# Kernel tuning notes

Measured on AMD Instinct MI355X. Metric: run time of the kernel, lower is better.

## Reference

```python
import jax, jax.numpy as jnp
import numpy as np

N = 50000
E = 800000
F_IN = 64
HID = 64
NCLS = 16


def setup_inputs() -> dict:
    key = jax.random.key(0)
    ks = jax.random.split(key, 8)
    x = jax.random.normal(ks[0], (N, F_IN), dtype=jnp.float32)
    edge_index = jax.random.randint(ks[1], (2, E), 0, N, dtype=jnp.int64)
    edge_weight = jax.random.uniform(ks[2], (E,), dtype=jnp.float32)
    # GCNConv glorot-style weights (PyG stores weight as [in, out]) and zero bias
    W1 = jax.random.normal(ks[3], (F_IN, HID), dtype=jnp.float32) * (1.0 / np.sqrt(F_IN))
    b1 = jnp.zeros((HID,), dtype=jnp.float32)
    W2 = jax.random.normal(ks[4], (HID, HID), dtype=jnp.float32) * (1.0 / np.sqrt(HID))
    b2 = jnp.zeros((HID,), dtype=jnp.float32)
    Wout = jax.random.normal(ks[5], (HID, NCLS), dtype=jnp.float32) * (1.0 / np.sqrt(HID))
    bout = jnp.zeros((NCLS,), dtype=jnp.float32)
    return {"x": x, "edge_index": edge_index, "edge_weight": edge_weight,
            "W1": W1, "b1": b1, "W2": W2, "b2": b2, "Wout": Wout, "bout": bout}


def _gcn_norm(edge_index, edge_weight, num_nodes):
    # PyG gcn_norm with add_self_loops=True (self-loop weight = 1.0)
    row = jnp.concatenate([edge_index[0], jnp.arange(num_nodes, dtype=edge_index.dtype)])
    col = jnp.concatenate([edge_index[1], jnp.arange(num_nodes, dtype=edge_index.dtype)])
    w = jnp.concatenate([edge_weight, jnp.ones((num_nodes,), dtype=edge_weight.dtype)])
    deg = jax.ops.segment_sum(w, col, num_segments=num_nodes)  # [N]
    dinv = jnp.where(deg > 0, jax.lax.rsqrt(deg), 0.0)
    norm = dinv[row] * w * dinv[col]  # [E+N]
    return row, col, norm


def _gcn_conv(h, row, col, norm, W, b, num_nodes):
    h = h @ W                                   # [N, out]
    msg = h[row] * norm[:, None]                # gather + scale, [E+N, out]
    out = jax.ops.segment_sum(msg, col, num_segments=num_nodes)  # scatter-add
    return out + b


def reference(x, edge_index, edge_weight, W1, b1, W2, b2, Wout, bout):
    num_nodes = x.shape[0]
    row, col, norm = _gcn_norm(edge_index, edge_weight, num_nodes)
    h = _gcn_conv(x, row, col, norm, W1, b1, num_nodes)
    h = jax.nn.relu(h)  # dropout is identity in eval mode
    h = _gcn_conv(h, row, col, norm, W2, b2, num_nodes)
    h = jax.nn.relu(h)
    logits = h @ Wout + bout
    return jax.nn.softmax(logits, axis=1)
```

## Files before the change

### kernel.cpp

```cpp
#include <hip/hip_runtime.h>
#include <math.h>

#define NN 50000
#define NE 800000
#define F 64
#define NCLS 16

#define BKS 7
#define BKN 128
#define NBK 391
#define CAP 2560
#define B1C 4096
#define B1B 196
#define CAP2 3072

typedef unsigned short u16;
typedef __attribute__((ext_vector_type(8))) unsigned short ushort8v;

__device__ __forceinline__ float bf2f(u16 h) {
    return __uint_as_float((unsigned)h << 16);
}
__device__ __forceinline__ u16 f2bf(float f) {
    unsigned u = __float_as_uint(f);
    return (u16)((u + 0x7fffu + ((u >> 16) & 1u)) >> 16);
}

__global__ void k_init_cur(int* __restrict__ cur) {
    int b = blockIdx.x * 256 + threadIdx.x;
    if (b < NBK) cur[b] = b * CAP;
}


__global__ __launch_bounds__(512) void k_bucket1(const int* __restrict__ row,
                                                 const int* __restrict__ col,
                                                 const float* __restrict__ w,
                                                 int* __restrict__ bkcur,
                                                 int2* __restrict__ tmp) {
    __shared__ int hist[512];
    __shared__ int sa[512], sb[512];
    __shared__ int lbase[512];
    __shared__ int gbase[512];
    __shared__ int lcur[512];
    __shared__ int2 stage[B1C];
    int t = threadIdx.x;
    int e0 = blockIdx.x * B1C;
    int cnt = min(B1C, NE - e0);
    hist[t] = 0;
    __syncthreads();

    int mykey[8]; int myb[8]; int myw[8]; bool myv[8];
#pragma unroll
    for (int k = 0; k < 8; ++k) {
        int i = t + k * 512;
        myv[k] = (i < cnt);
        if (myv[k]) {
            int e = e0 + i;
            int c = col[e];
            myb[k]   = c >> BKS;
            mykey[k] = (row[e] << BKS) | (c & (BKN - 1));
            myw[k]   = __float_as_int(w[e]);
            atomicAdd(&hist[myb[k]], 1);
        }
    }
    __syncthreads();

    sa[t] = hist[t];
    __syncthreads();
    int* src = sa; int* dst = sb;
#pragma unroll
    for (int off = 1; off < 512; off <<= 1) {
        dst[t] = src[t] + ((t >= off) ? src[t - off] : 0);
        __syncthreads();
        int* tq = src; src = dst; dst = tq;
    }
    int lex = src[t] - hist[t];
    lbase[t] = lex;
    lcur[t]  = lex;
    gbase[t] = (t < NBK && hist[t] > 0) ? atomicAdd(&bkcur[t], hist[t]) : 0;
    __syncthreads();

#pragma unroll
    for (int k = 0; k < 8; ++k) {
        if (myv[k]) {
            int pos = atomicAdd(&lcur[myb[k]], 1);
            stage[pos] = make_int2(mykey[k], myw[k]);
        }
    }
    __syncthreads();

    for (int i = t; i < cnt; i += 512) {
        int lo = 0, hi = NBK;
        while (hi - lo > 1) {
            int mid = (lo + hi) >> 1;
            if (lbase[mid] <= i) lo = mid; else hi = mid;
        }
        tmp[gbase[lo] + (i - lbase[lo])] = stage[i];
    }
}


__global__ __launch_bounds__(256) void k_bucket2(const int* __restrict__ bkcur,
                                                 const int2* __restrict__ tmp,
                                                 int2* __restrict__ sedge,
                                                 int* __restrict__ begA,
                                                 int* __restrict__ endA,
                                                 float* __restrict__ dinv) {
    __shared__ int2 stage[CAP2];
    __shared__ int2 sorted[CAP2];
    __shared__ int hist[BKN];
    __shared__ int sa[BKN], sb[BKN];
    __shared__ int lcur[BKN];
    int b = blockIdx.x;
    int t = threadIdx.x;
    int rbeg = b * CAP;
    int cnt = min(bkcur[b] - rbeg, CAP2);
    if (t < BKN) hist[t] = 0;
    __syncthreads();
    for (int i = t; i < cnt; i += 256) {
        int2 ed = tmp[rbeg + i];
        stage[i] = ed;
        atomicAdd(&hist[ed.x & (BKN - 1)], 1);
    }
    __syncthreads();
    if (t < BKN) sa[t] = hist[t];
    __syncthreads();
    int* src = sa; int* dst = sb;
#pragma unroll
    for (int off = 1; off < BKN; off <<= 1) {
        if (t < BKN) dst[t] = src[t] + ((t >= off) ? src[t - off] : 0);
        __syncthreads();
        int* tq = src; src = dst; dst = tq;
    }
    int node0 = b * BKN;
    int lincl = 0, lexcl = 0;
    if (t < BKN) {
        lincl = src[t];
        lexcl = lincl - hist[t];
        lcur[t] = lexcl;
        if (node0 + t < NN) {
            begA[node0 + t] = rbeg + lexcl;
            endA[node0 + t] = rbeg + lincl;
        }
    }
    __syncthreads();
    for (int i = t; i < cnt; i += 256) {
        int2 ed = stage[i];
        int pos = atomicAdd(&lcur[ed.x & (BKN - 1)], 1);
        sorted[pos] = ed;
    }
    __syncthreads();
    if (t < BKN && node0 + t < NN) {
        float s = 1.0f;
        for (int e = lexcl; e < lincl; ++e) s += __int_as_float(sorted[e].y);
        dinv[node0 + t] = rsqrtf(s);
    }
    for (int i = t; i < cnt; i += 256) {
        int2 ed = sorted[i];
        sedge[rbeg + i] = make_int2(ed.x >> BKS, ed.y);
    }
}


template<bool BF>
__global__ __launch_bounds__(256) void k_mm64(const void* __restrict__ Xv,
                                              const float* __restrict__ W,
                                              u16* __restrict__ Y) {
    __shared__ float sW[64 * 64];
    __shared__ float sX[16][64];
    int tid = threadIdx.x;
    int c  = tid & 63;
    int wv = tid >> 6;
    for (int i = tid; i < 64 * 64; i += 256) sW[i] = W[i];
    int r0 = blockIdx.x * 16;
#pragma unroll
    for (int i = tid; i < 16 * 64; i += 256) {
        size_t idx = (size_t)(r0 + (i >> 6)) * 64 + (i & 63);
        if (BF) sX[i >> 6][i & 63] = bf2f(((const u16*)Xv)[idx]);
        else    sX[i >> 6][i & 63] = ((const float*)Xv)[idx];
    }
    __syncthreads();
    int rb = wv * 4;
    float a0 = 0.f, a1 = 0.f, a2 = 0.f, a3 = 0.f;
#pragma unroll
    for (int k = 0; k < 64; k += 4) {
        float4 x0 = *(const float4*)&sX[rb + 0][k];
        float4 x1 = *(const float4*)&sX[rb + 1][k];
        float4 x2 = *(const float4*)&sX[rb + 2][k];
        float4 x3 = *(const float4*)&sX[rb + 3][k];
        float wA = sW[(k + 0) * 64 + c];
        float wB = sW[(k + 1) * 64 + c];
        float wC = sW[(k + 2) * 64 + c];
        float wD = sW[(k + 3) * 64 + c];
        a0 += x0.x * wA + x0.y * wB + x0.z * wC + x0.w * wD;
        a1 += x1.x * wA + x1.y * wB + x1.z * wC + x1.w * wD;
        a2 += x2.x * wA + x2.y * wB + x2.z * wC + x2.w * wD;
        a3 += x3.x * wA + x3.y * wB + x3.z * wC + x3.w * wD;
    }
    Y[(size_t)(r0 + rb + 0) * 64 + c] = f2bf(a0);
    Y[(size_t)(r0 + rb + 1) * 64 + c] = f2bf(a1);
    Y[(size_t)(r0 + rb + 2) * 64 + c] = f2bf(a2);
    Y[(size_t)(r0 + rb + 3) * 64 + c] = f2bf(a3);
}


template<bool HEAD>
__global__ __launch_bounds__(256) void k_agg(const u16* __restrict__ A,
                                             const int* __restrict__ begA,
                                             const int* __restrict__ endA,
                                             const int2* __restrict__ sedge,
                                             const float* __restrict__ dinv,
                                             const float* __restrict__ bias,
                                             u16* __restrict__ B,
                                             const float* __restrict__ Wout,
                                             const float* __restrict__ bout,
                                             float* __restrict__ out) {
    __shared__ float sWout[64 * NCLS];
    __shared__ float sh[8][64];
    int tid  = threadIdx.x;
    int wv   = tid >> 6;
    int lane = tid & 63;
    int half = lane >> 5;
    int sub  = lane & 31;
    int slot = sub >> 3;
    int fg   = sub & 7;
    int node = blockIdx.x * 8 + wv * 2 + half;
    if (HEAD) {
        for (int i = tid; i < 64 * NCLS; i += 256) sWout[i] = Wout[i];
    }
    int beg = begA[node];
    int deg = endA[node] - beg;
    float acc[8] = {0.f, 0.f, 0.f, 0.f, 0.f, 0.f, 0.f, 0.f};
    for (int base = 0; base < deg; base += 32) {
        int i = base + sub;
        int2 ed = (i < deg) ? sedge[beg + i] : make_int2(0, 0);
        float nmr = __int_as_float(ed.y) * dinv[ed.x];
        int m = min(32, deg - base);
        int steps = (m + 3) >> 2;
        for (int t = 0; t < steps; ++t) {
            int idx = (half << 5) + (t << 2) + slot;
            int   s  = __shfl(ed.x, idx);
            float nm = __shfl(nmr, idx);
            const ushort8v a = *(const ushort8v*)(A + (size_t)s * 64 + (fg << 3));
#pragma unroll
            for (int j = 0; j < 8; ++j) acc[j] += bf2f(a[j]) * nm;
        }
    }
#pragma unroll
    for (int o = 8; o <= 16; o <<= 1) {
#pragma unroll
        for (int j = 0; j < 8; ++j) acc[j] += __shfl_xor(acc[j], o);
    }
    if (slot == 0) {
        float d = dinv[node];
        float d2 = d * d;
        const ushort8v self = *(const ushort8v*)(A + (size_t)node * 64 + (fg << 3));
        const float4 bb0 = *(const float4*)(bias + (fg << 3));
        const float4 bb1 = *(const float4*)(bias + (fg << 3) + 4);
        float bbv[8] = {bb0.x, bb0.y, bb0.z, bb0.w, bb1.x, bb1.y, bb1.z, bb1.w};
        ushort8v ov;
#pragma unroll
        for (int j = 0; j < 8; ++j) {
            float v = fmaxf(acc[j] * d + bf2f(self[j]) * d2 + bbv[j], 0.f);
            ov[j] = f2bf(v);
            if (HEAD) sh[wv * 2 + half][(fg << 3) + j] = v;
        }
        *(ushort8v*)(B + (size_t)node * 64 + (fg << 3)) = ov;
    }
    if (HEAD) {
        __syncthreads();
        int nib  = tid >> 5;
        int sub2 = tid & 31;
        int c = sub2 & 15, q = sub2 >> 4;
        const float* hrow = sh[nib];
        float p = 0.f;
#pragma unroll
        for (int k = 0; k < 32; ++k)
            p += hrow[q * 32 + k] * sWout[(q * 32 + k) * NCLS + c];
        p += __shfl_xor(p, 16);
        p += bout[c];
        float mx = p;
#pragma unroll
        for (int o = 8; o >= 1; o >>= 1) mx = fmaxf(mx, __shfl_xor(mx, o, 16));
        float ex = expf(p - mx);
        float s = ex;
#pragma unroll
        for (int o = 8; o >= 1; o >>= 1) s += __shfl_xor(s, o, 16);
        if (q == 0) out[(size_t)(blockIdx.x * 8 + nib) * NCLS + c] = ex / s;
    }
}


extern "C" void kernel_launch(void* const* d_in, const int* in_sizes, int n_in,
                              void* d_out, int out_size, void* d_ws, size_t ws_size,
                              hipStream_t stream) {
    const float* x    = (const float*)d_in[0];
    const int*   ei   = (const int*)d_in[1];
    const float* ew   = (const float*)d_in[2];
    const float* W1   = (const float*)d_in[3];
    const float* b1   = (const float*)d_in[4];
    const float* W2   = (const float*)d_in[5];
    const float* b2   = (const float*)d_in[6];
    const float* Wout = (const float*)d_in[7];
    const float* bout = (const float*)d_in[8];
    const int* row = ei;
    const int* col = ei + NE;

    int*   ip     = (int*)d_ws;
    int*   begA   = ip;
    int*   endA   = ip + 50048;
    float* dinv   = (float*)(ip + 100096);
    int*   bkcur  = ip + 150144;
    int2*  sedge  = (int2*)(ip + 150656);
    u16*   A      = (u16*)(ip + 150656 + 2 * NBK * CAP);
    u16*   B      = A + 3200000;
    int2*  tmp    = (int2*)A;

    k_init_cur<<<2, 256, 0, stream>>>(bkcur);
    k_bucket1<<<B1B, 512, 0, stream>>>(row, col, ew, bkcur, tmp);
    k_bucket2<<<NBK, 256, 0, stream>>>(bkcur, tmp, sedge, begA, endA, dinv);

    k_mm64<false><<<NN / 16, 256, 0, stream>>>(x, W1, A);
    k_agg<false><<<NN / 8, 256, 0, stream>>>(A, begA, endA, sedge, dinv, b1, B,
                                             nullptr, nullptr, nullptr);
    k_mm64<true><<<NN / 16, 256, 0, stream>>>(B, W2, A);
    k_agg<true><<<NN / 8, 256, 0, stream>>>(A, begA, endA, sedge, dinv, b2, B,
                                            Wout, bout, (float*)d_out);
}
```

Measured before the change: 188.2 us.

## Fuse first-layer matmul into edge bucketing kernel and peel first aggregation chunk

```diff
diff --git a/kernel.cpp b/kernel.cpp
--- a/kernel.cpp
+++ b/kernel.cpp
@@ -12,6 +12,7 @@
 #define CAP 2560
 #define B1C 4096
 #define B1B 196
+#define MMB 1563
 #define CAP2 3072
 
 typedef unsigned short u16;
@@ -31,70 +32,112 @@
 }
 
 
-__global__ __launch_bounds__(512) void k_bucket1(const int* __restrict__ row,
+__global__ __launch_bounds__(512) void k_sort_mm(const int* __restrict__ row,
                                                  const int* __restrict__ col,
                                                  const float* __restrict__ w,
                                                  int* __restrict__ bkcur,
-                                                 int2* __restrict__ tmp) {
-    __shared__ int hist[512];
-    __shared__ int sa[512], sb[512];
-    __shared__ int lbase[512];
-    __shared__ int gbase[512];
-    __shared__ int lcur[512];
-    __shared__ int2 stage[B1C];
+                                                 int2* __restrict__ tmp,
+                                                 const float* __restrict__ X,
+                                                 const float* __restrict__ W,
+                                                 u16* __restrict__ Y) {
+    __shared__ __align__(16) char smem[53248];
     int t = threadIdx.x;
-    int e0 = blockIdx.x * B1C;
-    int cnt = min(B1C, NE - e0);
-    hist[t] = 0;
-    __syncthreads();
-
-    int mykey[8]; int myb[8]; int myw[8]; bool myv[8];
-#pragma unroll
-    for (int k = 0; k < 8; ++k) {
-        int i = t + k * 512;
-        myv[k] = (i < cnt);
-        if (myv[k]) {
-            int e = e0 + i;
-            int c = col[e];
-            myb[k]   = c >> BKS;
-            mykey[k] = (row[e] << BKS) | (c & (BKN - 1));
-            myw[k]   = __float_as_int(w[e]);
-            atomicAdd(&hist[myb[k]], 1);
-        }
-    }
-    __syncthreads();
-
-    sa[t] = hist[t];
-    __syncthreads();
-    int* src = sa; int* dst = sb;
-#pragma unroll
-    for (int off = 1; off < 512; off <<= 1) {
-        dst[t] = src[t] + ((t >= off) ? src[t - off] : 0);
-        __syncthreads();
-        int* tq = src; src = dst; dst = tq;
-    }
-    int lex = src[t] - hist[t];
-    lbase[t] = lex;
-    lcur[t]  = lex;
-    gbase[t] = (t < NBK && hist[t] > 0) ? atomicAdd(&bkcur[t], hist[t]) : 0;
-    __syncthreads();
-
-#pragma unroll
-    for (int k = 0; k < 8; ++k) {
-        if (myv[k]) {
-            int pos = atomicAdd(&lcur[myb[k]], 1);
-            stage[pos] = make_int2(mykey[k], myw[k]);
-        }
-    }
-    __syncthreads();
-
-    for (int i = t; i < cnt; i += 512) {
-        int lo = 0, hi = NBK;
-        while (hi - lo > 1) {
-            int mid = (lo + hi) >> 1;
-            if (lbase[mid] <= i) lo = mid; else hi = mid;
-        }
-        tmp[gbase[lo] + (i - lbase[lo])] = stage[i];
+    if (blockIdx.x < B1B) {
+        int*  hist   = (int*)smem;
+        int*  sa     = hist + 512;
+        int*  sb     = sa + 512;
+        int*  lbase  = sb + 512;
+        int*  gbase  = lbase + 512;
+        int*  lcur   = gbase + 512;
+        u16*  stageB = (u16*)(lcur + 512);
+        int2* stage  = (int2*)(stageB + 4096);
+
+        int e0 = blockIdx.x * B1C;
+        int cnt = min(B1C, NE - e0);
+        hist[t] = 0;
+        __syncthreads();
+
+        int mykey[8]; int myb[8]; int myw[8]; bool myv[8];
+#pragma unroll
+        for (int k = 0; k < 8; ++k) {
+            int i = t + k * 512;
+            myv[k] = (i < cnt);
+            if (myv[k]) {
+                int e = e0 + i;
+                int c = col[e];
+                myb[k]   = c >> BKS;
+                mykey[k] = (row[e] << BKS) | (c & (BKN - 1));
+                myw[k]   = __float_as_int(w[e]);
+                atomicAdd(&hist[myb[k]], 1);
+            }
+        }
+        __syncthreads();
+
+        sa[t] = hist[t];
+        __syncthreads();
+        int* src = sa; int* dst = sb;
+#pragma unroll
+        for (int off = 1; off < 512; off <<= 1) {
+            dst[t] = src[t] + ((t >= off) ? src[t - off] : 0);
+            __syncthreads();
+            int* tq = src; src = dst; dst = tq;
+        }
+        int lex = src[t] - hist[t];
+        lbase[t] = lex;
+        lcur[t]  = lex;
+        gbase[t] = (t < NBK && hist[t] > 0) ? atomicAdd(&bkcur[t], hist[t]) : 0;
+        __syncthreads();
+
+#pragma unroll
+        for (int k = 0; k < 8; ++k) {
+            if (myv[k]) {
+                int pos = atomicAdd(&lcur[myb[k]], 1);
+                stage[pos]  = make_int2(mykey[k], myw[k]);
+                stageB[pos] = (u16)myb[k];
+            }
+        }
+        __syncthreads();
+
+        for (int i = t; i < cnt; i += 512) {
+            int b = stageB[i];
+            tmp[gbase[b] + (i - lbase[b])] = stage[i];
+        }
+    } else {
+        float* sW = (float*)smem;
+        float (*sX)[64] = (float(*)[64])(smem + 16384);
+        for (int i = t; i < 64 * 64; i += 512) sW[i] = W[i];
+        int r0 = (blockIdx.x - B1B) * 32;
+        for (int i = t; i < 32 * 64; i += 512) {
+            int rr = i >> 6, cc = i & 63;
+            int r = r0 + rr;
+            sX[rr][cc] = (r < NN) ? X[(size_t)r * 64 + cc] : 0.f;
+        }
+        __syncthreads();
+        int c  = t & 63;
+        int wv = t >> 6;
+        int rb = wv * 4;
+        float a0 = 0.f, a1 = 0.f, a2 = 0.f, a3 = 0.f;
+#pragma unroll
+        for (int k = 0; k < 64; k += 4) {
+            float4 x0 = *(const float4*)&sX[rb + 0][k];
+            float4 x1 = *(const float4*)&sX[rb + 1][k];
+            float4 x2 = *(const float4*)&sX[rb + 2][k];
+            float4 x3 = *(const float4*)&sX[rb + 3][k];
+            float wA = sW[(k + 0) * 64 + c];
+            float wB = sW[(k + 1) * 64 + c];
+            float wC = sW[(k + 2) * 64 + c];
+            float wD = sW[(k + 3) * 64 + c];
+            a0 += x0.x * wA + x0.y * wB + x0.z * wC + x0.w * wD;
+            a1 += x1.x * wA + x1.y * wB + x1.z * wC + x1.w * wD;
+            a2 += x2.x * wA + x2.y * wB + x2.z * wC + x2.w * wD;
+            a3 += x3.x * wA + x3.y * wB + x3.z * wC + x3.w * wD;
+        }
+        float av[4] = {a0, a1, a2, a3};
+#pragma unroll
+        for (int k = 0; k < 4; ++k) {
+            int r = r0 + rb + k;
+            if (r < NN) Y[(size_t)r * 64 + c] = f2bf(av[k]);
+        }
     }
 }
 
@@ -161,10 +204,9 @@
 }
 
 
-template<bool BF>
-__global__ __launch_bounds__(256) void k_mm64(const void* __restrict__ Xv,
-                                              const float* __restrict__ W,
-                                              u16* __restrict__ Y) {
+__global__ __launch_bounds__(256) void k_mm64b(const u16* __restrict__ Xv,
+                                               const float* __restrict__ W,
+                                               u16* __restrict__ Y) {
     __shared__ float sW[64 * 64];
     __shared__ float sX[16][64];
     int tid = threadIdx.x;
@@ -175,8 +217,7 @@
 #pragma unroll
     for (int i = tid; i < 16 * 64; i += 256) {
         size_t idx = (size_t)(r0 + (i >> 6)) * 64 + (i & 63);
-        if (BF) sX[i >> 6][i & 63] = bf2f(((const u16*)Xv)[idx]);
-        else    sX[i >> 6][i & 63] = ((const float*)Xv)[idx];
+        sX[i >> 6][i & 63] = bf2f(Xv[idx]);
     }
     __syncthreads();
     int rb = wv * 4;
@@ -230,7 +271,24 @@
     int beg = begA[node];
     int deg = endA[node] - beg;
     float acc[8] = {0.f, 0.f, 0.f, 0.f, 0.f, 0.f, 0.f, 0.f};
-    for (int base = 0; base < deg; base += 32) {
+
+    {
+        int2 ed = (sub < deg) ? sedge[beg + sub] : make_int2(0, 0);
+        float nmr = __int_as_float(ed.y) * dinv[ed.x];
+        int mval = min(32, deg);
+#pragma unroll
+        for (int t = 0; t < 8; ++t) {
+            if ((t << 2) < mval) {
+                int idx = (half << 5) + (t << 2) + slot;
+                int   s  = __shfl(ed.x, idx);
+                float nm = __shfl(nmr, idx);
+                const ushort8v a = *(const ushort8v*)(A + (size_t)s * 64 + (fg << 3));
+#pragma unroll
+                for (int j = 0; j < 8; ++j) acc[j] += bf2f(a[j]) * nm;
+            }
+        }
+    }
+    for (int base = 32; base < deg; base += 32) {
         int i = base + sub;
         int2 ed = (i < deg) ? sedge[beg + i] : make_int2(0, 0);
         float nmr = __int_as_float(ed.y) * dinv[ed.x];
@@ -311,18 +369,17 @@
     float* dinv   = (float*)(ip + 100096);
     int*   bkcur  = ip + 150144;
     int2*  sedge  = (int2*)(ip + 150656);
-    u16*   A      = (u16*)(ip + 150656 + 2 * NBK * CAP);
+    int2*  tmp    = sedge + (size_t)NBK * CAP;
+    u16*   A      = (u16*)(tmp + (size_t)NBK * CAP);
     u16*   B      = A + 3200000;
-    int2*  tmp    = (int2*)A;
 
     k_init_cur<<<2, 256, 0, stream>>>(bkcur);
-    k_bucket1<<<B1B, 512, 0, stream>>>(row, col, ew, bkcur, tmp);
+    k_sort_mm<<<B1B + MMB, 512, 0, stream>>>(row, col, ew, bkcur, tmp, x, W1, A);
     k_bucket2<<<NBK, 256, 0, stream>>>(bkcur, tmp, sedge, begA, endA, dinv);
 
-    k_mm64<false><<<NN / 16, 256, 0, stream>>>(x, W1, A);
     k_agg<false><<<NN / 8, 256, 0, stream>>>(A, begA, endA, sedge, dinv, b1, B,
                                              nullptr, nullptr, nullptr);
-    k_mm64<true><<<NN / 16, 256, 0, stream>>>(B, W2, A);
+    k_mm64b<<<NN / 16, 256, 0, stream>>>(B, W2, A);
     k_agg<true><<<NN / 8, 256, 0, stream>>>(A, begA, endA, sedge, dinv, b2, B,
                                             Wout, bout, (float*)d_out);
 }
```

New measurement: 202.0 us. 7.4% more time.
